# Optimization experiments

Hardware: AMD Instinct MI355X
Metric: run time of the kernel (lower is better)

Reference implementation:

```python
import jax, jax.numpy as jnp
import numpy as np

# Model / simulation constants (mirror EvNN __init__ static fields)
N_NEURONS = 4096
IN_SIZE = 1024
K_SPIKES = 8
T0 = 0.0
MAX_TIME = 1.0
DT = 0.01                 # solver_stepsize (Euler, ConstantStepSize)
N_STEPS = 100             # ceil(MAX_TIME / DT)
DLIM = 0.05               # max synaptic delay
D_BINS = 5                # ceil(DLIM / DT): circular delay-buffer depth
TAU = 0.1                 # LIF membrane time constant
V_TH = 1.0                # spike threshold (event / root condition)
V_RESET = 0.0


def setup_inputs() -> dict:
    key = jax.random.key(0)
    k1, k2, k3 = jax.random.split(key, 3)
    in_spike_times = jax.random.uniform(k1, (IN_SIZE, K_SPIKES), minval=0.0, maxval=MAX_TIME, dtype=jnp.float32)
    # W rows: [0:N_NEURONS] recurrent synapses, [N_NEURONS:] input synapses
    W = jax.random.normal(k2, (N_NEURONS + IN_SIZE, N_NEURONS), dtype=jnp.float32) * (1.5 / np.sqrt(N_NEURONS))
    delays = jax.random.uniform(k3, (N_NEURONS + IN_SIZE, N_NEURONS), minval=0.0, maxval=DLIM, dtype=jnp.float32)
    return {"in_spike_times": in_spike_times, "W": W, "delays": delays}


def reference(in_spike_times, W, delays):
    n = N_NEURONS
    # --- input spike -> delayed arrival scatter (EvNN.init_buffer) ---
    W_in = W[n:]                              # [M, N]
    d_in = jnp.maximum(delays[n:], 0.0)       # [M, N]
    t_arr = in_spike_times[:, :, None] + d_in[:, None, :]      # [M, K, N] arrival times
    bins = jnp.floor((t_arr - T0) / DT).astype(jnp.int32)      # time bin per delivery
    valid = (bins >= 0) & (bins < N_STEPS)
    bins = jnp.clip(bins, 0, N_STEPS - 1)
    contrib = jnp.where(valid, jnp.broadcast_to(W_in[:, None, :], t_arr.shape), 0.0)
    col = jnp.broadcast_to(jnp.arange(n, dtype=jnp.int32)[None, None, :], t_arr.shape)
    I_in = jnp.zeros((N_STEPS, n), W.dtype).at[bins.ravel(), col.ravel()].add(contrib.ravel())

    # --- recurrent delay bins (delivery >= next step, like the spike buffer) ---
    W_rec = W[:n]                             # [N, N]
    dbin = jnp.clip(jnp.floor(jnp.maximum(delays[:n], 0.0) / DT).astype(jnp.int32) + 1, 1, D_BINS)
    col_rec = jnp.broadcast_to(jnp.arange(n, dtype=jnp.int32)[None, :], (n, n))

    decay = jnp.asarray(DT / TAU, W.dtype)

    def step(carry, I_ext):
        v, buf, t = carry
        slot = t % D_BINS
        I = I_ext + buf[slot]
        v_new = v + decay * (-v) + I          # explicit Euler on dv/dt = -v/tau + I/dt
        spike = (v_new >= V_TH).astype(W.dtype)   # event detection (threshold crossing)
        v_out = jnp.where(spike > 0, jnp.asarray(V_RESET, W.dtype), v_new)
        buf = buf.at[slot].set(0.0)           # pop current buffer slot
        tgt = (t + dbin) % D_BINS             # [N, N] future delivery slot per synapse
        buf = buf.at[tgt, col_rec].add(spike[:, None] * W_rec)  # delay-buffer scatter
        return (v_out, buf, t + 1), v_out

    v0 = jnp.zeros((n,), W.dtype)
    buf0 = jnp.zeros((D_BINS, n), W.dtype)
    (_, _, _), v_trace = jax.lax.scan(step, (v0, buf0, jnp.int32(0)), I_in)
    return v_trace  # [N_STEPS, N_NEURONS] membrane trajectory of output neurons
```

## Files before the change

kernel.cpp:

```cpp
#include <hip/hip_runtime.h>
#include <hip/hip_cooperative_groups.h>
#include <math.h>

#pragma clang fp contract(off)

namespace cg = cooperative_groups;

#define N      4096
#define INSZ   1024
#define KSP    8
#define NSTEP  100
#define NB     64
#define CPB    64
#define NCH    16
#define ICH    8
#define JG     32

__device__ float              g_I[NSTEP * N];
__device__ float              g_part[ICH * NSTEP * N];
__device__ unsigned char      g_dbin[(size_t)N * N];
__device__ unsigned long long g_pub[NSTEP * NB * 2];

__global__ __launch_bounds__(256) void k_prep(const float4* __restrict__ delays4) {
    int idx = blockIdx.x * 256 + threadIdx.x;
    int stride = gridDim.x * 256;
    for (int f = idx; f < NSTEP * NB * 2; f += stride) g_pub[f] = 0ull;
    const int tot4 = (N / 4) * N;
    for (int e = idx; e < tot4; e += stride) {
        float4 d4 = delays4[e];
        uchar4 o;
        { float d = fmaxf(d4.x, 0.0f); int db = (int)__fmul_rn(d, 100.0f) + 1; o.x = (unsigned char)(db > 5 ? 5 : db); }
        { float d = fmaxf(d4.y, 0.0f); int db = (int)__fmul_rn(d, 100.0f) + 1; o.y = (unsigned char)(db > 5 ? 5 : db); }
        { float d = fmaxf(d4.z, 0.0f); int db = (int)__fmul_rn(d, 100.0f) + 1; o.z = (unsigned char)(db > 5 ? 5 : db); }
        { float d = fmaxf(d4.w, 0.0f); int db = (int)__fmul_rn(d, 100.0f) + 1; o.w = (unsigned char)(db > 5 ? 5 : db); }
        *(uchar4*)&g_dbin[(size_t)e * 4] = o;
    }
}

__global__ __launch_bounds__(128) void k_input_part(const float* __restrict__ st,
                                                    const float* __restrict__ Wm,
                                                    const float* __restrict__ delays) {
    __shared__ float acc[NSTEP * 128];
    int jg = blockIdx.x & (JG - 1);
    int ic = blockIdx.x / JG;
    int tid = threadIdx.x;
    int j = jg * 128 + tid;
    for (int b = 0; b < NSTEP; b++) acc[b * 128 + tid] = 0.0f;
    __syncthreads();
    int i0 = ic * (INSZ / ICH);
    for (int ii = 0; ii < INSZ / ICH; ii++) {
        int i = i0 + ii;
        size_t base = (size_t)(N + i) * N + j;
        float d = fmaxf(delays[base], 0.0f);
        float w = Wm[base];
        const float* sp = st + i * KSP;
        #pragma unroll
        for (int k = 0; k < KSP; k++) {
            float tt = __fadd_rn(sp[k], d);
            float q  = __fmul_rn(tt, 100.0f);
            if (q < 100.0f) {
                int b = (int)q;
                atomicAdd(&acc[b * 128 + tid], w);
            }
        }
    }
    __syncthreads();
    for (int b = 0; b < NSTEP; b++)
        g_part[((size_t)ic * NSTEP + b) * N + j] = acc[b * 128 + tid];
}

__global__ __launch_bounds__(256) void k_input_red() {
    int idx = blockIdx.x * 256 + threadIdx.x;
    int stride = gridDim.x * 256;
    for (int e = idx; e < NSTEP * N; e += stride) {
        float s = 0.0f;
        #pragma unroll
        for (int c = 0; c < ICH; c++)
            s = __fadd_rn(s, g_part[(size_t)c * NSTEP * N + e]);
        g_I[e] = s;
    }
}

__global__ __launch_bounds__(256, 1) void k_sim(const float* __restrict__ Wm,
                                                float* __restrict__ out) {
    int tid  = threadIdx.x;
    int blk  = blockIdx.x;
    int lane = tid & 63;

    __shared__ float          pbuf[NCH * 5 * CPB];
    __shared__ float          I_lds[NSTEP * CPB];
    __shared__ unsigned short list[N];
    __shared__ int            s_cnt;

    for (int e = tid; e < NSTEP * CPB; e += 256) {
        int t = e >> 6, c = e & 63;
        I_lds[e] = g_I[t * N + blk * CPB + c];
    }
    for (int e = tid; e < NCH * 5 * CPB; e += 256) pbuf[e] = 0.0f;
    __syncthreads();

    int quad  = tid & (NCH - 1);
    int chunk = tid >> 4;
    int col0  = blk * CPB + quad * 4;
    float v = 0.0f;

    for (int t = 0; t < NSTEP; t++) {
        int slot = t % 5;
        unsigned long long expseq = (unsigned long long)(t + 1);

        if (tid < CPB) {
            float bufv = 0.0f;
            #pragma unroll
            for (int c = 0; c < NCH; c++) {
                int a = (c * 5 + slot) * CPB + tid;
                bufv = __fadd_rn(bufv, pbuf[a]);
                pbuf[a] = 0.0f;
            }
            float I  = __fadd_rn(I_lds[t * CPB + tid], bufv);
            float vn = __fadd_rn(__fadd_rn(v, __fmul_rn(0.1f, -v)), I);
            bool  spk = (vn >= 1.0f);
            float vo = spk ? 0.0f : vn;
            v = vo;
            unsigned long long m = __ballot(spk);
            if (tid == 0) {
                unsigned long long w0 = ((m & 0xFFFFFFFFull) << 32) | expseq;
                unsigned long long w1 = ((m >> 32) << 32) | expseq;
                __hip_atomic_store(&g_pub[(t * NB + blk) * 2 + 0], w0,
                                   __ATOMIC_RELAXED, __HIP_MEMORY_SCOPE_AGENT);
                __hip_atomic_store(&g_pub[(t * NB + blk) * 2 + 1], w1,
                                   __ATOMIC_RELAXED, __HIP_MEMORY_SCOPE_AGENT);
            }
            out[t * N + blk * CPB + tid] = vo;
        } else if (tid < 128) {
            unsigned long long w0, w1;
            do {
                w0 = __hip_atomic_load(&g_pub[(t * NB + lane) * 2 + 0],
                                       __ATOMIC_RELAXED, __HIP_MEMORY_SCOPE_AGENT);
            } while ((unsigned)w0 != (unsigned)expseq);
            do {
                w1 = __hip_atomic_load(&g_pub[(t * NB + lane) * 2 + 1],
                                       __ATOMIC_RELAXED, __HIP_MEMORY_SCOPE_AGENT);
            } while ((unsigned)w1 != (unsigned)expseq);
            unsigned long long mm = (w0 >> 32) | ((w1 >> 32) << 32);

            int pc = __popcll(mm);
            int incl = pc;
            #pragma unroll
            for (int o = 1; o < 64; o <<= 1) {
                int nbv = __shfl_up(incl, o, 64);
                if (lane >= o) incl += nbv;
            }
            int off = incl - pc;
            if (lane == 63) s_cnt = incl;
            while (mm) {
                int bb = __builtin_ctzll(mm);
                mm &= mm - 1;
                list[off++] = (unsigned short)((lane << 6) + bb);
            }
        }
        __syncthreads();

        int S  = s_cnt;
        int lo = (S * chunk) >> 4;
        int hi = (S * (chunk + 1)) >> 4;
        float* pb = &pbuf[chunk * 5 * CPB];
        int cb = quad * 4;
        #pragma unroll 4
        for (int s = lo; s < hi; s++) {
            int i = (int)list[s];
            size_t base = (size_t)i * N + col0;
            float4 w4 = *(const float4*)&Wm[base];
            uchar4 d4 = *(const uchar4*)&g_dbin[base];
            int r0 = slot + d4.x; if (r0 >= 5) r0 -= 5;
            int r1 = slot + d4.y; if (r1 >= 5) r1 -= 5;
            int r2 = slot + d4.z; if (r2 >= 5) r2 -= 5;
            int r3 = slot + d4.w; if (r3 >= 5) r3 -= 5;
            atomicAdd(&pb[r0 * CPB + cb + 0], w4.x);
            atomicAdd(&pb[r1 * CPB + cb + 1], w4.y);
            atomicAdd(&pb[r2 * CPB + cb + 2], w4.z);
            atomicAdd(&pb[r3 * CPB + cb + 3], w4.w);
        }
        __syncthreads();
    }
}

extern "C" void kernel_launch(void* const* d_in, const int* in_sizes, int n_in,
                              void* d_out, int out_size, void* d_ws, size_t ws_size,
                              hipStream_t stream) {
    const float* st     = (const float*)d_in[0];
    const float* Wm     = (const float*)d_in[1];
    const float* delays = (const float*)d_in[2];
    float* out = (float*)d_out;

    k_prep      <<<256, 256, 0, stream>>>((const float4*)delays);
    k_input_part<<<JG * ICH, 128, 0, stream>>>(st, Wm, delays);
    k_input_red <<<256, 256, 0, stream>>>();

    void* args[] = { (void*)&Wm, (void*)&out };
    hipLaunchCooperativeKernel((const void*)k_sim, dim3(NB), dim3(256),
                               args, 0, stream);
}
```

Measured before the change: 1.432 ms.

## Consolidate simulation into 16 large blocks with per-wave spike publishing

```diff
diff --git a/kernel.cpp b/kernel.cpp
--- a/kernel.cpp
+++ b/kernel.cpp
@@ -1,30 +1,28 @@
 #include <hip/hip_runtime.h>
-#include <hip/hip_cooperative_groups.h>
 #include <math.h>
 
 #pragma clang fp contract(off)
-
-namespace cg = cooperative_groups;
 
 #define N      4096
 #define INSZ   1024
 #define KSP    8
 #define NSTEP  100
-#define NB     64
-#define CPB    64
+#define NBS    16
+#define CPB    256
 #define NCH    16
+#define NGRP   64
 #define ICH    8
 #define JG     32
 
 __device__ float              g_I[NSTEP * N];
 __device__ float              g_part[ICH * NSTEP * N];
 __device__ unsigned char      g_dbin[(size_t)N * N];
-__device__ unsigned long long g_pub[NSTEP * NB * 2];
+__device__ unsigned long long g_pub[NSTEP * NGRP * 2];
 
 __global__ __launch_bounds__(256) void k_prep(const float4* __restrict__ delays4) {
     int idx = blockIdx.x * 256 + threadIdx.x;
     int stride = gridDim.x * 256;
-    for (int f = idx; f < NSTEP * NB * 2; f += stride) g_pub[f] = 0ull;
+    for (int f = idx; f < NSTEP * NGRP * 2; f += stride) g_pub[f] = 0ull;
     const int tot4 = (N / 4) * N;
     for (int e = idx; e < tot4; e += stride) {
         float4 d4 = delays4[e];
@@ -81,26 +79,24 @@
     }
 }
 
-__global__ __launch_bounds__(256, 1) void k_sim(const float* __restrict__ Wm,
-                                                float* __restrict__ out) {
+__global__ __launch_bounds__(1024, 1) void k_sim(const float* __restrict__ Wm,
+                                                 float* __restrict__ out) {
     int tid  = threadIdx.x;
     int blk  = blockIdx.x;
     int lane = tid & 63;
+    int wave = tid >> 6;
 
     __shared__ float          pbuf[NCH * 5 * CPB];
-    __shared__ float          I_lds[NSTEP * CPB];
+    __shared__ float          Ibuf[2][CPB];
     __shared__ unsigned short list[N];
     __shared__ int            s_cnt;
 
-    for (int e = tid; e < NSTEP * CPB; e += 256) {
-        int t = e >> 6, c = e & 63;
-        I_lds[e] = g_I[t * N + blk * CPB + c];
-    }
-    for (int e = tid; e < NCH * 5 * CPB; e += 256) pbuf[e] = 0.0f;
+    for (int e = tid; e < NCH * 5 * CPB; e += 1024) pbuf[e] = 0.0f;
+    if (tid < CPB) Ibuf[0][tid] = g_I[0 * N + blk * CPB + tid];
     __syncthreads();
 
-    int quad  = tid & (NCH - 1);
-    int chunk = tid >> 4;
+    int quad  = tid & 63;
+    int chunk = tid >> 6;
     int col0  = blk * CPB + quad * 4;
     float v = 0.0f;
 
@@ -116,29 +112,30 @@
                 bufv = __fadd_rn(bufv, pbuf[a]);
                 pbuf[a] = 0.0f;
             }
-            float I  = __fadd_rn(I_lds[t * CPB + tid], bufv);
+            float I  = __fadd_rn(Ibuf[t & 1][tid], bufv);
             float vn = __fadd_rn(__fadd_rn(v, __fmul_rn(0.1f, -v)), I);
             bool  spk = (vn >= 1.0f);
             float vo = spk ? 0.0f : vn;
             v = vo;
             unsigned long long m = __ballot(spk);
-            if (tid == 0) {
+            if (lane == 0) {
+                int g = blk * 4 + wave;
                 unsigned long long w0 = ((m & 0xFFFFFFFFull) << 32) | expseq;
                 unsigned long long w1 = ((m >> 32) << 32) | expseq;
-                __hip_atomic_store(&g_pub[(t * NB + blk) * 2 + 0], w0,
+                __hip_atomic_store(&g_pub[(t * NGRP + g) * 2 + 0], w0,
                                    __ATOMIC_RELAXED, __HIP_MEMORY_SCOPE_AGENT);
-                __hip_atomic_store(&g_pub[(t * NB + blk) * 2 + 1], w1,
+                __hip_atomic_store(&g_pub[(t * NGRP + g) * 2 + 1], w1,
                                    __ATOMIC_RELAXED, __HIP_MEMORY_SCOPE_AGENT);
             }
             out[t * N + blk * CPB + tid] = vo;
-        } else if (tid < 128) {
+        } else if (wave == 4) {
             unsigned long long w0, w1;
             do {
-                w0 = __hip_atomic_load(&g_pub[(t * NB + lane) * 2 + 0],
+                w0 = __hip_atomic_load(&g_pub[(t * NGRP + lane) * 2 + 0],
                                        __ATOMIC_RELAXED, __HIP_MEMORY_SCOPE_AGENT);
             } while ((unsigned)w0 != (unsigned)expseq);
             do {
-                w1 = __hip_atomic_load(&g_pub[(t * NB + lane) * 2 + 1],
+                w1 = __hip_atomic_load(&g_pub[(t * NGRP + lane) * 2 + 1],
                                        __ATOMIC_RELAXED, __HIP_MEMORY_SCOPE_AGENT);
             } while ((unsigned)w1 != (unsigned)expseq);
             unsigned long long mm = (w0 >> 32) | ((w1 >> 32) << 32);
@@ -156,6 +153,11 @@
                 int bb = __builtin_ctzll(mm);
                 mm &= mm - 1;
                 list[off++] = (unsigned short)((lane << 6) + bb);
+            }
+        } else if (wave == 5) {
+            if (t + 1 < NSTEP) {
+                float4 iv = *(const float4*)&g_I[(t + 1) * N + blk * CPB + lane * 4];
+                *(float4*)&Ibuf[(t + 1) & 1][lane * 4] = iv;
             }
         }
         __syncthreads();
@@ -195,8 +197,5 @@
     k_prep      <<<256, 256, 0, stream>>>((const float4*)delays);
     k_input_part<<<JG * ICH, 128, 0, stream>>>(st, Wm, delays);
     k_input_red <<<256, 256, 0, stream>>>();
-
-    void* args[] = { (void*)&Wm, (void*)&out };
-    hipLaunchCooperativeKernel((const void*)k_sim, dim3(NB), dim3(256),
-                               args, 0, stream);
-}
+    k_sim       <<<NBS, 1024, 0, stream>>>(Wm, out);
+}
```

After: 3.882 ms. 171% more time.
